# Performance work log

Measured on AMD Instinct MI355X. Metric: run time of the kernel, lower is better.

## Reference

```python
import jax, jax.numpy as jnp
import numpy as np

BQ, BK = 128, 64  # SpargeAttn-style Q/K block sizes
NEG = -1e30


def _block_mask(q, k, simthreshd1, cdfthreshd, scale):
    """Mean-similarity block selection: a (q-block, k-block) pair is pruned only
    when both blocks are self-similar (mean cosine sim to block mean exceeds the
    per-head simthreshd1) AND it is not in the top-CDF mass (cdfthreshd) of the
    compressed block-level softmax."""
    B, H, L, D = q.shape
    nq, nk = L // BQ, L // BK
    qb = q.reshape(B, H, nq, BQ, D)
    kb = k.reshape(B, H, nk, BK, D)
    qm = qb.mean(3)  # [B,H,nq,D] block means
    km = kb.mean(3)  # [B,H,nk,D]

    def blocksim(xb, xm):
        xn = xb / (jnp.linalg.norm(xb, axis=-1, keepdims=True) + 1e-6)
        mn = xm / (jnp.linalg.norm(xm, axis=-1, keepdims=True) + 1e-6)
        return jnp.einsum('bhntd,bhnd->bhnt', xn, mn).mean(-1)  # [B,H,n]

    th = simthreshd1[None, :, None]
    comp_q = blocksim(qb, qm) > th  # [B,H,nq] self-similar q blocks
    comp_k = blocksim(kb, km) > th  # [B,H,nk]

    # compressed attention over block means, then CDF-based top-mass selection
    p = jax.nn.softmax(jnp.einsum('bhqd,bhkd->bhqk', qm, km) * scale, axis=-1)
    order = jnp.argsort(-p, axis=-1)
    sp = jnp.take_along_axis(p, order, axis=-1)
    csum = jnp.cumsum(sp, axis=-1)
    keep_sorted = (csum - sp) < cdfthreshd[None, :, None, None]  # prefix covering tau
    rank = jnp.argsort(order, axis=-1)  # inverse permutation
    selected = jnp.take_along_axis(keep_sorted, rank, axis=-1)  # [B,H,nq,nk]

    return selected | ~(comp_q[..., :, None] & comp_k[..., None, :])


def setup_inputs() -> dict:
    key = jax.random.key(0)
    kq, kk, kv, kc = jax.random.split(key, 4)
    B, H, L, D = 1, 16, 2048, 64
    return {
        'q': jax.random.normal(kq, (B, H, L, D), dtype=jnp.float32),
        'k': jax.random.normal(kk, (B, H, L, D), dtype=jnp.float32),
        'v': jax.random.normal(kv, (B, H, L, D), dtype=jnp.float32),
        'simthreshd1': jnp.zeros((H,), dtype=jnp.float32),
        'cdfthreshd': jax.random.uniform(kc, (H,), dtype=jnp.float32),
    }


def reference(q, k, v, simthreshd1, cdfthreshd):
    B, H, L, D = q.shape
    scale = 1.0 / np.sqrt(D).astype(np.float32)
    # smooth_k: subtract per-(B,H) key mean (softmax-invariant shift, matches kernel)
    k = k - k.mean(axis=-2, keepdims=True)
    bmask = _block_mask(q, k, simthreshd1, cdfthreshd, scale)  # [B,H,nq,nk] bool
    mask_tok = jnp.repeat(jnp.repeat(bmask, BQ, axis=2), BK, axis=3)  # [B,H,L,L]
    s = jnp.einsum('bhqd,bhkd->bhqk', q, k) * scale
    s = jnp.where(mask_tok, s, NEG)
    p = jax.nn.softmax(s, axis=-1)
    return jnp.einsum('bhqk,bhkd->bhqd', p, v)
```

## Files before the change

kernel.cpp:

```cpp
#include <hip/hip_runtime.h>

#define HH 16
#define LL 2048
#define DD 64
#define BQ 128
#define BK 64
#define NQ (LL/BQ)
#define NK (LL/BK)
#define SCALE 0.125f
#define QSCALE (0.125f * 1.44269504f)

typedef __attribute__((ext_vector_type(8))) short s8v;
typedef __attribute__((ext_vector_type(4))) float f4v;

static __device__ __forceinline__ ushort f2bf(float x) {
    unsigned u = __float_as_uint(x);
    u += 0x7fff + ((u >> 16) & 1);
    return (ushort)(u >> 16);
}

__global__ void kmean1_kernel(const float* __restrict__ k, float* __restrict__ kpart) {
    int b = blockIdx.x;
    int h = blockIdx.y;
    int t = threadIdx.x;
    int d = t & 63, c = t >> 6;
    const float* kh = k + ((size_t)h*LL + (size_t)b*256) * DD;
    float s = 0.f;
    for (int l = c*64; l < c*64 + 64; ++l) s += kh[(size_t)l * DD + d];
    __shared__ float red[4][64];
    red[c][d] = s;
    __syncthreads();
    if (t < 64) kpart[((size_t)h*8 + b)*64 + t] = red[0][t]+red[1][t]+red[2][t]+red[3][t];
}

__global__ __launch_bounds__(128) void stats_kernel(
        const float* __restrict__ q, const float* __restrict__ k, const float* __restrict__ v,
        const float* __restrict__ kpart, const float* __restrict__ simth,
        float* __restrict__ qm, float* __restrict__ km,
        int* __restrict__ compq, int* __restrict__ compk,
        ushort* __restrict__ qb, ushort* __restrict__ kb, ushort* __restrict__ vTb) {
    __shared__ __align__(16) char smem[34304];
    int h = blockIdx.y, t = threadIdx.x;

    if ((int)blockIdx.x < NQ) {
        int qi = blockIdx.x;
        float (*xs)[DD+1] = (float(*)[DD+1])smem;
        float* mean = (float*)(smem + 33280);
        float* red  = (float*)(smem + 33536);
        size_t row = (size_t)h*LL + (size_t)qi*BQ + t;
        const float* rp = q + row * DD;
        float x[DD]; float n2 = 0.f;
        #pragma unroll
        for (int d = 0; d < DD; d += 4) {
            float4 v4 = *(const float4*)(rp + d);
            x[d]=v4.x; x[d+1]=v4.y; x[d+2]=v4.z; x[d+3]=v4.w;
            n2 += v4.x*v4.x + v4.y*v4.y + v4.z*v4.z + v4.w*v4.w;
        }
        #pragma unroll
        for (int d = 0; d < DD; d += 4) {
            ushort4 o;
            o.x = f2bf(x[d]*QSCALE);   o.y = f2bf(x[d+1]*QSCALE);
            o.z = f2bf(x[d+2]*QSCALE); o.w = f2bf(x[d+3]*QSCALE);
            *(ushort4*)(qb + row*DD + d) = o;
        }
        #pragma unroll
        for (int d = 0; d < DD; ++d) xs[t][d] = x[d];
        __syncthreads();
        if (t < DD) {
            float s = 0.f;
            for (int r = 0; r < BQ; ++r) s += xs[r][t];
            mean[t] = s * (1.0f/BQ);
        }
        __syncthreads();
        float dot = 0.f, m2 = 0.f;
        #pragma unroll
        for (int d = 0; d < DD; ++d) { dot += x[d]*mean[d]; m2 += mean[d]*mean[d]; }
        float cs = dot / ((sqrtf(n2) + 1e-6f) * (sqrtf(m2) + 1e-6f));
        red[t] = cs; __syncthreads();
        for (int sft = BQ/2; sft > 0; sft >>= 1) {
            if (t < sft) red[t] += red[t + sft];
            __syncthreads();
        }
        if (t == 0) compq[h*NQ + qi] = (red[0] * (1.0f/BQ)) > simth[h] ? 1 : 0;
        if (t < DD) qm[((size_t)h*NQ + qi)*DD + t] = mean[t];
    } else {
        int ki = blockIdx.x - NQ;
        float* mu_s = (float*)smem;
        float (*xs)[DD+1] = (float(*)[DD+1])(smem + 256);
        ushort (*vs)[66]  = (ushort(*)[66])(smem + 256 + 16640);
        float* mean = (float*)(smem + 256 + 16640 + 8448);
        float* red  = (float*)(smem + 256 + 16640 + 8448 + 256);
        if (t < 64) {
            float s = 0.f;
            #pragma unroll
            for (int b = 0; b < 8; ++b) s += kpart[((size_t)h*8 + b)*64 + t];
            mu_s[t] = s * (1.0f/LL);
        }
        __syncthreads();
        size_t rowb = (size_t)h*LL + (size_t)ki*BK;
        float x[DD]; float n2 = 0.f;
        if (t < 64) {
            const float* rp = k + (rowb + t) * DD;
            #pragma unroll
            for (int d = 0; d < DD; d += 4) {
                float4 v4 = *(const float4*)(rp + d);
                v4.x -= mu_s[d]; v4.y -= mu_s[d+1]; v4.z -= mu_s[d+2]; v4.w -= mu_s[d+3];
                x[d]=v4.x; x[d+1]=v4.y; x[d+2]=v4.z; x[d+3]=v4.w;
                n2 += v4.x*v4.x + v4.y*v4.y + v4.z*v4.z + v4.w*v4.w;
            }
            #pragma unroll
            for (int d = 0; d < DD; d += 4) {
                ushort4 o;
                o.x = f2bf(x[d]);   o.y = f2bf(x[d+1]);
                o.z = f2bf(x[d+2]); o.w = f2bf(x[d+3]);
                *(ushort4*)(kb + (rowb + t)*DD + d) = o;
            }
            #pragma unroll
            for (int d = 0; d < DD; ++d) xs[t][d] = x[d];
        } else {
            int tk = t - 64;
            const float* vp = v + (rowb + tk) * DD;
            #pragma unroll
            for (int d = 0; d < DD; d += 4) {
                float4 v4 = *(const float4*)(vp + d);
                vs[tk][d]   = f2bf(v4.x); vs[tk][d+1] = f2bf(v4.y);
                vs[tk][d+2] = f2bf(v4.z); vs[tk][d+3] = f2bf(v4.w);
            }
        }
        __syncthreads();
        if (t < 64) {
            size_t vbase = ((size_t)h*DD + t)*LL + (size_t)ki*64;
            #pragma unroll
            for (int r8 = 0; r8 < 64; r8 += 8) {
                s8v o;
                #pragma unroll
                for (int e = 0; e < 8; ++e) o[e] = (short)vs[r8+e][t];
                *(s8v*)(vTb + vbase + r8) = o;
            }
            float s = 0.f;
            for (int r = 0; r < BK; ++r) s += xs[r][t];
            mean[t] = s * (1.0f/BK);
        }
        __syncthreads();
        if (t < 64) {
            float dot = 0.f, m2 = 0.f;
            #pragma unroll
            for (int d = 0; d < DD; ++d) { dot += x[d]*mean[d]; m2 += mean[d]*mean[d]; }
            float cs = dot / ((sqrtf(n2) + 1e-6f) * (sqrtf(m2) + 1e-6f));
            red[t] = cs;
        }
        __syncthreads();
        for (int sft = 32; sft > 0; sft >>= 1) {
            if (t < sft) red[t] += red[t + sft];
            __syncthreads();
        }
        if (t == 0) compk[h*NK + ki] = (red[0] * (1.0f/BK)) > simth[h] ? 1 : 0;
        if (t < 64) km[((size_t)h*NK + ki)*DD + t] = mean[t];
    }
}

__global__ void bmask_kernel(const float* __restrict__ qm, const float* __restrict__ km,
                             const int* __restrict__ compq, const int* __restrict__ compk,
                             const float* __restrict__ cdfth, unsigned* __restrict__ bmaskbits) {
    int qi = blockIdx.x, h = blockIdx.y;
    int j = threadIdx.x;
    __shared__ float ssh[NK];
    __shared__ float p[NK];
    const float* qv = qm + ((size_t)h*NQ + qi)*DD;
    const float* kv = km + ((size_t)h*NK + j)*DD;
    float s = 0.f;
    for (int d = 0; d < DD; ++d) s += qv[d]*kv[d];
    ssh[j] = s * SCALE;
    __syncthreads();
    float m = ssh[0];
    for (int i = 1; i < NK; ++i) m = fmaxf(m, ssh[i]);
    float den = 0.f;
    for (int i = 0; i < NK; ++i) den += expf(ssh[i] - m);
    p[j] = expf(ssh[j] - m) / den;
    __syncthreads();
    float pj = p[j];
    float mass = 0.f;
    for (int i = 0; i < NK; ++i) {
        float pi = p[i];
        if (pi > pj || (pi == pj && i < j)) mass += pi;
    }
    int sel = (mass < cdfth[h]) ? 1 : 0;
    int keep = (sel || !(compq[h*NQ+qi] && compk[h*NK+j])) ? 1 : 0;
    unsigned long long bal = __ballot(keep);
    if (j == 0) bmaskbits[h*NQ + qi] = (unsigned)bal;
}

__global__ __launch_bounds__(256, 2) void attn_kernel(
        const ushort* __restrict__ qb, const ushort* __restrict__ kb,
        const ushort* __restrict__ vTb, const unsigned* __restrict__ bmaskbits,
        float* __restrict__ out) {
    __shared__ __align__(16) char shmem[69632];
    ushort* pl = (ushort*)(shmem) + (threadIdx.x >> 6) * 64 * 80;
    float*  Ob = (float*)shmem;
    float*  mb = (float*)(shmem + 67584);
    float*  lb = (float*)(shmem + 68608);

    int h    = blockIdx.y;
    int qi   = blockIdx.x >> 1;
    int half = blockIdx.x & 1;
    int tid  = threadIdx.x;
    int w    = tid >> 6;
    int l    = tid & 63;
    int lo = l & 15, hi = l >> 4;
    int r0 = qi*BQ + half*64;

    unsigned msk = bmaskbits[h*NQ + qi];

    const ushort* qh = qb  + (size_t)h*LL*DD;
    const ushort* kh = kb  + (size_t)h*LL*DD;
    const ushort* vh = vTb + (size_t)h*DD*LL;

    s8v qf[4][2];
    #pragma unroll
    for (int qt = 0; qt < 4; ++qt)
        #pragma unroll
        for (int kk = 0; kk < 2; ++kk)
            qf[qt][kk] = *(const s8v*)(qh + (size_t)(r0 + qt*16 + lo)*DD + kk*32 + hi*8);

    f4v O[4][4];
    float m[4], lsum[4];
    #pragma unroll
    for (int qt = 0; qt < 4; ++qt) {
        m[qt] = -1e30f; lsum[qt] = 0.f;
        #pragma unroll
        for (int dt = 0; dt < 4; ++dt) O[qt][dt] = (f4v){0.f,0.f,0.f,0.f};
    }

    unsigned mm = msk; int rank = 0;
    while (mm) {
        int j = __ffs(mm) - 1; mm &= mm - 1;
        if (((rank++) & 3) != w) continue;

        const ushort* kbj = kh + (size_t)j*BK*DD;
        const ushort* vbj = vh + (size_t)j*BK;

        s8v kf[4][2];
        #pragma unroll
        for (int kt = 0; kt < 4; ++kt)
            #pragma unroll
            for (int kk = 0; kk < 2; ++kk)
                kf[kt][kk] = *(const s8v*)(kbj + (size_t)(kt*16 + lo)*DD + kk*32 + hi*8);

        f4v S[4][4];
        #pragma unroll
        for (int kt = 0; kt < 4; ++kt)
            #pragma unroll
            for (int qt = 0; qt < 4; ++qt)
                S[kt][qt] = (f4v){0.f,0.f,0.f,0.f};
        __builtin_amdgcn_s_setprio(1);
        #pragma unroll
        for (int kk = 0; kk < 2; ++kk)
            #pragma unroll
            for (int kt = 0; kt < 4; ++kt)
                #pragma unroll
                for (int qt = 0; qt < 4; ++qt)
                    S[kt][qt] = __builtin_amdgcn_mfma_f32_16x16x32_bf16(kf[kt][kk], qf[qt][kk], S[kt][qt], 0, 0, 0);
        __builtin_amdgcn_s_setprio(0);

        s8v vf[2][4];
        #pragma unroll
        for (int kk = 0; kk < 2; ++kk)
            #pragma unroll
            for (int dt = 0; dt < 4; ++dt)
                vf[kk][dt] = *(const s8v*)(vbj + (size_t)(dt*16 + lo)*LL + kk*32 + hi*8);

        float pm[4];
        #pragma unroll
        for (int qt = 0; qt < 4; ++qt) {
            float a0 = fmaxf(fmaxf(S[0][qt][0],S[0][qt][1]), fmaxf(S[0][qt][2],S[0][qt][3]));
            float a1 = fmaxf(fmaxf(S[1][qt][0],S[1][qt][1]), fmaxf(S[1][qt][2],S[1][qt][3]));
            float a2 = fmaxf(fmaxf(S[2][qt][0],S[2][qt][1]), fmaxf(S[2][qt][2],S[2][qt][3]));
            float a3 = fmaxf(fmaxf(S[3][qt][0],S[3][qt][1]), fmaxf(S[3][qt][2],S[3][qt][3]));
            float p = fmaxf(fmaxf(a0,a1), fmaxf(a2,a3));
            p = fmaxf(p, __shfl_xor(p, 16));
            p = fmaxf(p, __shfl_xor(p, 32));
            pm[qt] = p;
        }
        bool grow = (pm[0] > m[0]+8.0f) | (pm[1] > m[1]+8.0f) |
                    (pm[2] > m[2]+8.0f) | (pm[3] > m[3]+8.0f);
        if (__any(grow)) {
            float alpha[4];
            #pragma unroll
            for (int qt = 0; qt < 4; ++qt) {
                float mn = fmaxf(m[qt], pm[qt]);
                alpha[qt] = __builtin_amdgcn_exp2f(m[qt] - mn);
                lsum[qt] *= alpha[qt];
                m[qt] = mn;
            }
            #pragma unroll
            for (int qt = 0; qt < 4; ++qt)
                #pragma unroll
                for (int r = 0; r < 4; ++r) {
                    float a = __shfl(alpha[qt], hi*4 + r);
                    #pragma unroll
                    for (int dt = 0; dt < 4; ++dt) O[qt][dt][r] *= a;
                }
        }
        #pragma unroll
        for (int qt = 0; qt < 4; ++qt) {
            float ps = 0.f;
            #pragma unroll
            for (int kt = 0; kt < 4; ++kt) {
                float p0 = __builtin_amdgcn_exp2f(S[kt][qt][0] - m[qt]);
                float p1 = __builtin_amdgcn_exp2f(S[kt][qt][1] - m[qt]);
                float p2 = __builtin_amdgcn_exp2f(S[kt][qt][2] - m[qt]);
                float p3 = __builtin_amdgcn_exp2f(S[kt][qt][3] - m[qt]);
                ps += (p0 + p1) + (p2 + p3);
                unsigned c01, c23;
                asm("v_cvt_pk_bf16_f32 %0, %1, %2" : "=v"(c01) : "v"(p0), "v"(p1));
                asm("v_cvt_pk_bf16_f32 %0, %1, %2" : "=v"(c23) : "v"(p2), "v"(p3));
                *(uint2*)&pl[(qt*16 + lo)*80 + kt*16 + hi*4] = make_uint2(c01, c23);
            }
            lsum[qt] += ps;
        }
        __builtin_amdgcn_s_setprio(1);
        #pragma unroll
        for (int qt = 0; qt < 4; ++qt)
            #pragma unroll
            for (int kk = 0; kk < 2; ++kk) {
                s8v pa = *(const s8v*)&pl[(qt*16 + lo)*80 + kk*32 + hi*8];
                #pragma unroll
                for (int dt = 0; dt < 4; ++dt)
                    O[qt][dt] = __builtin_amdgcn_mfma_f32_16x16x32_bf16(pa, vf[kk][dt], O[qt][dt], 0, 0, 0);
            }
        __builtin_amdgcn_s_setprio(0);
    }

    #pragma unroll
    for (int qt = 0; qt < 4; ++qt) {
        lsum[qt] += __shfl_xor(lsum[qt], 16);
        lsum[qt] += __shfl_xor(lsum[qt], 32);
    }

    __syncthreads();

    if (hi == 0) {
        #pragma unroll
        for (int qt = 0; qt < 4; ++qt) {
            mb[w*64 + qt*16 + lo] = m[qt];
            lb[w*64 + qt*16 + lo] = lsum[qt];
        }
    }
    #pragma unroll
    for (int qt = 0; qt < 4; ++qt)
        #pragma unroll
        for (int dt = 0; dt < 4; ++dt)
            #pragma unroll
            for (int r = 0; r < 4; ++r)
                Ob[w*4224 + (qt*16 + hi*4 + r)*66 + dt*16 + lo] = O[qt][dt][r];
    __syncthreads();

    {
        int q = l;
        float mw0 = mb[q], mw1 = mb[64+q], mw2 = mb[128+q], mw3 = mb[192+q];
        float ms = fmaxf(fmaxf(mw0,mw1), fmaxf(mw2,mw3));
        float c0 = __builtin_amdgcn_exp2f(mw0 - ms);
        float c1 = __builtin_amdgcn_exp2f(mw1 - ms);
        float c2 = __builtin_amdgcn_exp2f(mw2 - ms);
        float c3 = __builtin_amdgcn_exp2f(mw3 - ms);
        float ls = lb[q]*c0 + lb[64+q]*c1 + lb[128+q]*c2 + lb[192+q]*c3;
        float inv = 1.0f / ls;
        float* orow = out + ((size_t)h*LL + r0 + q)*DD + w*16;
        #pragma unroll
        for (int i4 = 0; i4 < 4; ++i4) {
            float4 o;
            #pragma unroll
            for (int e = 0; e < 4; ++e) {
                int d = w*16 + i4*4 + e;
                float acc = Ob[q*66 + d]*c0 + Ob[4224 + q*66 + d]*c1
                          + Ob[8448 + q*66 + d]*c2 + Ob[12672 + q*66 + d]*c3;
                ((float*)&o)[e] = acc * inv;
            }
            *(float4*)(orow + i4*4) = o;
        }
    }
}

extern "C" void kernel_launch(void* const* d_in, const int* in_sizes, int n_in,
                              void* d_out, int out_size, void* d_ws, size_t ws_size,
                              hipStream_t stream) {
    const float* q     = (const float*)d_in[0];
    const float* k     = (const float*)d_in[1];
    const float* v     = (const float*)d_in[2];
    const float* simth = (const float*)d_in[3];
    const float* cdfth = (const float*)d_in[4];
    float* out = (float*)d_out;

    float* ws    = (float*)d_ws;
    float* kpart = ws;
    float* qm    = kpart + HH*8*64;
    float* km    = qm + HH*NQ*DD;
    int*   compq = (int*)(km + HH*NK*DD);
    int*   compk = compq + HH*NQ;
    unsigned* bmb = (unsigned*)(compk + HH*NK);
    size_t off = (size_t)((char*)(bmb + HH*NQ) - (char*)d_ws);
    off = (off + 15) & ~(size_t)15;
    ushort* qbuf = (ushort*)((char*)d_ws + off);
    ushort* kbuf = qbuf + (size_t)HH*LL*DD;
    ushort* vTb  = kbuf + (size_t)HH*LL*DD;

    kmean1_kernel<<<dim3(8, HH), 256, 0, stream>>>(k, kpart);
    stats_kernel<<<dim3(NQ + NK, HH), 128, 0, stream>>>(q, k, v, kpart, simth,
                                                        qm, km, compq, compk,
                                                        qbuf, kbuf, vTb);
    bmask_kernel<<<dim3(NQ, HH), NK, 0, stream>>>(qm, km, compq, compk, cdfth, bmb);
    attn_kernel<<<dim3(NQ*2, HH), 256, 0, stream>>>(qbuf, kbuf, vTb, bmb, out);
}
```

Measured before the change: 75.28 us.

## Fuse block-mask selection into attention kernel and tweak stats and MFMA scheduling

Removes the separate bmask kernel launch. Each attention wavefront now computes the block-level softmax and CDF selection itself, using width-32 wave shuffles. It also splits the q-block mean reduction across all 128 threads, moves the V fragment loads ahead of the QK MFMAs, drops the s_setprio hints, and shrinks the P staging row stride from 80 to 72. The mask computation is now repeated redundantly by every wave of every block, and the new LDS stride may change bank-conflict behaviour.

Measured after the change: 74.37 us. About the same (-1.2%).

```diff
diff --git a/kernel.cpp b/kernel.cpp
--- a/kernel.cpp
+++ b/kernel.cpp
@@ -66,16 +66,20 @@
         #pragma unroll
         for (int d = 0; d < DD; ++d) xs[t][d] = x[d];
         __syncthreads();
-        if (t < DD) {
+        {
+            int d = t & 63, hf = t >> 6;
             float s = 0.f;
-            for (int r = 0; r < BQ; ++r) s += xs[r][t];
-            mean[t] = s * (1.0f/BQ);
-        }
+            for (int r = hf*64; r < hf*64 + 64; ++r) s += xs[r][d];
+            red[t] = s;
+        }
+        __syncthreads();
+        if (t < DD) mean[t] = (red[t] + red[64 + t]) * (1.0f/BQ);
         __syncthreads();
         float dot = 0.f, m2 = 0.f;
         #pragma unroll
         for (int d = 0; d < DD; ++d) { dot += x[d]*mean[d]; m2 += mean[d]*mean[d]; }
         float cs = dot / ((sqrtf(n2) + 1e-6f) * (sqrtf(m2) + 1e-6f));
+        __syncthreads();
         red[t] = cs; __syncthreads();
         for (int sft = BQ/2; sft > 0; sft >>= 1) {
             if (t < sft) red[t] += red[t + sft];
@@ -159,43 +163,14 @@
     }
 }
 
-__global__ void bmask_kernel(const float* __restrict__ qm, const float* __restrict__ km,
-                             const int* __restrict__ compq, const int* __restrict__ compk,
-                             const float* __restrict__ cdfth, unsigned* __restrict__ bmaskbits) {
-    int qi = blockIdx.x, h = blockIdx.y;
-    int j = threadIdx.x;
-    __shared__ float ssh[NK];
-    __shared__ float p[NK];
-    const float* qv = qm + ((size_t)h*NQ + qi)*DD;
-    const float* kv = km + ((size_t)h*NK + j)*DD;
-    float s = 0.f;
-    for (int d = 0; d < DD; ++d) s += qv[d]*kv[d];
-    ssh[j] = s * SCALE;
-    __syncthreads();
-    float m = ssh[0];
-    for (int i = 1; i < NK; ++i) m = fmaxf(m, ssh[i]);
-    float den = 0.f;
-    for (int i = 0; i < NK; ++i) den += expf(ssh[i] - m);
-    p[j] = expf(ssh[j] - m) / den;
-    __syncthreads();
-    float pj = p[j];
-    float mass = 0.f;
-    for (int i = 0; i < NK; ++i) {
-        float pi = p[i];
-        if (pi > pj || (pi == pj && i < j)) mass += pi;
-    }
-    int sel = (mass < cdfth[h]) ? 1 : 0;
-    int keep = (sel || !(compq[h*NQ+qi] && compk[h*NK+j])) ? 1 : 0;
-    unsigned long long bal = __ballot(keep);
-    if (j == 0) bmaskbits[h*NQ + qi] = (unsigned)bal;
-}
-
 __global__ __launch_bounds__(256, 2) void attn_kernel(
         const ushort* __restrict__ qb, const ushort* __restrict__ kb,
-        const ushort* __restrict__ vTb, const unsigned* __restrict__ bmaskbits,
-        float* __restrict__ out) {
+        const ushort* __restrict__ vTb,
+        const float* __restrict__ qm, const float* __restrict__ km,
+        const int* __restrict__ compq, const int* __restrict__ compk,
+        const float* __restrict__ cdfth, float* __restrict__ out) {
     __shared__ __align__(16) char shmem[69632];
-    ushort* pl = (ushort*)(shmem) + (threadIdx.x >> 6) * 64 * 80;
+    ushort* pl = (ushort*)shmem + (threadIdx.x >> 6) * 64 * 72;
     float*  Ob = (float*)shmem;
     float*  mb = (float*)(shmem + 67584);
     float*  lb = (float*)(shmem + 68608);
@@ -209,7 +184,31 @@
     int lo = l & 15, hi = l >> 4;
     int r0 = qi*BQ + half*64;
 
-    unsigned msk = bmaskbits[h*NQ + qi];
+    unsigned msk;
+    {
+        int j = l & 31;
+        const float* qv = qm + ((size_t)h*NQ + qi)*DD;
+        const float* kv = km + ((size_t)h*NK + j)*DD;
+        float s = 0.f;
+        #pragma unroll
+        for (int d = 0; d < DD; ++d) s += qv[d]*kv[d];
+        s *= SCALE;
+        float mx = s;
+        #pragma unroll
+        for (int xm = 1; xm <= 16; xm <<= 1) mx = fmaxf(mx, __shfl_xor(mx, xm, 32));
+        float e = expf(s - mx);
+        float den = 0.f;
+        for (int i = 0; i < 32; ++i) den += __shfl(e, i, 32);
+        float p = e / den;
+        float mass = 0.f;
+        for (int i = 0; i < 32; ++i) {
+            float pi = __shfl(p, i, 32);
+            if (pi > p || (pi == p && i < j)) mass += pi;
+        }
+        int keep = (mass < cdfth[h]) || !(compq[h*NQ+qi] && compk[h*NK+j]);
+        unsigned long long bal = __ballot(keep != 0);
+        msk = (unsigned)bal;
+    }
 
     const ushort* qh = qb  + (size_t)h*LL*DD;
     const ushort* kh = kb  + (size_t)h*LL*DD;
@@ -246,13 +245,19 @@
             for (int kk = 0; kk < 2; ++kk)
                 kf[kt][kk] = *(const s8v*)(kbj + (size_t)(kt*16 + lo)*DD + kk*32 + hi*8);
 
+        s8v vf[2][4];
+        #pragma unroll
+        for (int kk = 0; kk < 2; ++kk)
+            #pragma unroll
+            for (int dt = 0; dt < 4; ++dt)
+                vf[kk][dt] = *(const s8v*)(vbj + (size_t)(dt*16 + lo)*LL + kk*32 + hi*8);
+
         f4v S[4][4];
         #pragma unroll
         for (int kt = 0; kt < 4; ++kt)
             #pragma unroll
             for (int qt = 0; qt < 4; ++qt)
                 S[kt][qt] = (f4v){0.f,0.f,0.f,0.f};
-        __builtin_amdgcn_s_setprio(1);
         #pragma unroll
         for (int kk = 0; kk < 2; ++kk)
             #pragma unroll
@@ -260,14 +265,6 @@
                 #pragma unroll
                 for (int qt = 0; qt < 4; ++qt)
                     S[kt][qt] = __builtin_amdgcn_mfma_f32_16x16x32_bf16(kf[kt][kk], qf[qt][kk], S[kt][qt], 0, 0, 0);
-        __builtin_amdgcn_s_setprio(0);
-
-        s8v vf[2][4];
-        #pragma unroll
-        for (int kk = 0; kk < 2; ++kk)
-            #pragma unroll
-            for (int dt = 0; dt < 4; ++dt)
-                vf[kk][dt] = *(const s8v*)(vbj + (size_t)(dt*16 + lo)*LL + kk*32 + hi*8);
 
         float pm[4];
         #pragma unroll
@@ -314,21 +311,19 @@
                 unsigned c01, c23;
                 asm("v_cvt_pk_bf16_f32 %0, %1, %2" : "=v"(c01) : "v"(p0), "v"(p1));
                 asm("v_cvt_pk_bf16_f32 %0, %1, %2" : "=v"(c23) : "v"(p2), "v"(p3));
-                *(uint2*)&pl[(qt*16 + lo)*80 + kt*16 + hi*4] = make_uint2(c01, c23);
+                *(uint2*)&pl[(qt*16 + lo)*72 + kt*16 + hi*4] = make_uint2(c01, c23);
             }
             lsum[qt] += ps;
         }
-        __builtin_amdgcn_s_setprio(1);
         #pragma unroll
         for (int qt = 0; qt < 4; ++qt)
             #pragma unroll
             for (int kk = 0; kk < 2; ++kk) {
-                s8v pa = *(const s8v*)&pl[(qt*16 + lo)*80 + kk*32 + hi*8];
+                s8v pa = *(const s8v*)&pl[(qt*16 + lo)*72 + kk*32 + hi*8];
                 #pragma unroll
                 for (int dt = 0; dt < 4; ++dt)
                     O[qt][dt] = __builtin_amdgcn_mfma_f32_16x16x32_bf16(pa, vf[kk][dt], O[qt][dt], 0, 0, 0);
             }
-        __builtin_amdgcn_s_setprio(0);
     }
 
     #pragma unroll
@@ -397,8 +392,7 @@
     float* km    = qm + HH*NQ*DD;
     int*   compq = (int*)(km + HH*NK*DD);
     int*   compk = compq + HH*NQ;
-    unsigned* bmb = (unsigned*)(compk + HH*NK);
-    size_t off = (size_t)((char*)(bmb + HH*NQ) - (char*)d_ws);
+    size_t off = (size_t)((char*)(compk + HH*NK) - (char*)d_ws);
     off = (off + 15) & ~(size_t)15;
     ushort* qbuf = (ushort*)((char*)d_ws + off);
     ushort* kbuf = qbuf + (size_t)HH*LL*DD;
@@ -408,6 +402,6 @@
     stats_kernel<<<dim3(NQ + NK, HH), 128, 0, stream>>>(q, k, v, kpart, simth,
                                                         qm, km, compq, compk,
                                                         qbuf, kbuf, vTb);
-    bmask_kernel<<<dim3(NQ, HH), NK, 0, stream>>>(qm, km, compq, compk, cdfth, bmb);
-    attn_kernel<<<dim3(NQ*2, HH), 256, 0, stream>>>(qbuf, kbuf, vTb, bmb, out);
+    attn_kernel<<<dim3(NQ*2, HH), 256, 0, stream>>>(qbuf, kbuf, vTb,
+                                                    qm, km, compq, compk, cdfth, out);
 }
```
